# Kernel optimization log

Measured on AMD Instinct MI355X. Metric: run time of the kernel, lower is better.

Reference implementation:

```python
import jax, jax.numpy as jnp
import numpy as np

H, W, D, C = 32, 16, 16, 4
NUM_ITERS = 2
THETA_GAMMA = 3.0   # spatial (position-only) kernel bandwidth
THETA_ALPHA = 8.0   # bilateral position bandwidth
THETA_BETA = 0.5    # bilateral color bandwidth


def _attn(feats, q):
    # Gaussian-kernel attention: softmax_j(-0.5 * ||f_i - f_j||^2) @ q
    # feats: [N, F], q: [N, C] -> [N, C]
    sq = jnp.sum(feats * feats, axis=-1)
    logits = feats @ feats.T - 0.5 * (sq[:, None] + sq[None, :])  # [N, N]
    return jax.nn.softmax(logits, axis=-1) @ q


def setup_inputs() -> dict:
    key = jax.random.key(0)
    k1, k2 = jax.random.split(key)
    unaries = jax.random.normal(k1, (1, H, W, D, C), dtype=jnp.float32)
    rgb = jax.random.normal(k2, (1, H, W, D, 3), dtype=jnp.float32)
    eye = jnp.eye(C, dtype=jnp.float32)
    return {
        "unaries": unaries,
        "rgb": rgb,
        "spatial_ker_weights": eye,          # _diagonal_initializer
        "bilateral_ker_weights": eye,        # _diagonal_initializer
        "compatibility_matrix": -eye,        # _potts_model_initializer
    }


def reference(unaries, rgb, spatial_ker_weights, bilateral_ker_weights, compatibility_matrix):
    N = H * W * D
    # positions start at 1 as in tf.range(1, h+1)
    grids = jnp.meshgrid(jnp.arange(1, H + 1), jnp.arange(1, W + 1), jnp.arange(1, D + 1), indexing='ij')
    pos = jnp.stack(grids, axis=-1).astype(jnp.float32).reshape(N, 3)
    rgb_flat = rgb.reshape(N, 3)
    spatial_feats = pos / THETA_GAMMA                                             # [N, 3]
    bilateral_feats = jnp.concatenate([pos / THETA_ALPHA, rgb_flat / THETA_BETA], axis=-1)  # [N, 6]

    u = unaries.reshape(N, C)
    q = u
    for _ in range(NUM_ITERS):
        sm = jax.nn.softmax(q, axis=-1)                         # [N, C]
        spatial_out = _attn(spatial_feats, sm)                  # [N, C]
        bilateral_out = _attn(bilateral_feats, sm)              # [N, C]
        # message_passing = SK @ spatial + BK @ bilateral (class-space matmul)
        message = spatial_out @ spatial_ker_weights.T + bilateral_out @ bilateral_ker_weights.T
        pairwise = message @ compatibility_matrix.T             # [N, C]
        q = u + pairwise
    return q.reshape(unaries.shape)
```

## Files before the change

kernel.cpp:

```cpp
#include <hip/hip_runtime.h>


#define HH 32
#define WW 16
#define DDD 16
#define NN (HH * WW * DDD)
#define KS 128
#define JC (NN / KS)
#define L2E 1.4426950408889634f
#define C18 (L2E / 18.0f)
#define SQL2E 1.2011224087864498f
#define SB (SQL2E / 8.0f)
#define SC (SQL2E / 0.5f)

#if __has_builtin(__builtin_amdgcn_exp2f)
#define EXP2(x) __builtin_amdgcn_exp2f(x)
#else
#define EXP2(x) exp2f(x)
#endif

__global__ __launch_bounds__(256) void conv_dw(
    const float* __restrict__ qin,
    float* __restrict__ tmp)
{
    int h = blockIdx.x;
    int s = threadIdx.x;
    int i = h * 256 + s;

    float4 q = *((const float4*)(qin + 4 * i));
    float m = fmaxf(fmaxf(q.x, q.y), fmaxf(q.z, q.w));
    float e0 = EXP2((q.x - m) * L2E), e1 = EXP2((q.y - m) * L2E);
    float e2 = EXP2((q.z - m) * L2E), e3 = EXP2((q.w - m) * L2E);
    float rs = 1.0f / (e0 + e1 + e2 + e3);

    __shared__ float A[256][4];
    __shared__ float B[256][4];
    *((float4*)A[s]) = make_float4(e0 * rs, e1 * rs, e2 * rs, e3 * rs);
    __syncthreads();

    int w = s >> 4, d = s & 15;
    float t0 = 0, t1 = 0, t2 = 0, t3 = 0;
    #pragma unroll
    for (int dp = 0; dp < DDD; ++dp) {
        float dd = (float)(d - dp);
        float k = EXP2(-dd * dd * C18);
        const float4 v = *((const float4*)A[w * 16 + dp]);
        t0 = fmaf(k, v.x, t0); t1 = fmaf(k, v.y, t1);
        t2 = fmaf(k, v.z, t2); t3 = fmaf(k, v.w, t3);
    }
    *((float4*)B[s]) = make_float4(t0, t1, t2, t3);
    __syncthreads();

    float u0 = 0, u1 = 0, u2 = 0, u3 = 0;
    #pragma unroll
    for (int wp = 0; wp < WW; ++wp) {
        float dw = (float)(w - wp);
        float k = EXP2(-dw * dw * C18);
        const float4 v = *((const float4*)B[wp * 16 + d]);
        u0 = fmaf(k, v.x, u0); u1 = fmaf(k, v.y, u1);
        u2 = fmaf(k, v.z, u2); u3 = fmaf(k, v.w, u3);
    }
    *((float4*)(tmp + 4 * i)) = make_float4(u0, u1, u2, u3);
}

__global__ __launch_bounds__(256) void bilat_pass1(
    const float* __restrict__ qin,
    const float* __restrict__ rgb,
    float* __restrict__ part)
{
    int ib = blockIdx.x >> 7;
    int kc = blockIdx.x & (KS - 1);
    int tid = threadIdx.x;
    int i0 = ib * 1024 + tid;
    int j0 = kc * JC;

    float fw = (float)(((tid >> 4) & 15) + 1) * SB;
    float fd = (float)((tid & 15) + 1) * SB;
    int hb = i0 >> 8;
    float fh[4], cr[4][3], nn[4];
    #pragma unroll
    for (int k = 0; k < 4; ++k) {
        int ik = i0 + k * 256;
        fh[k] = (float)(hb + k + 1) * SB;
        cr[k][0] = rgb[3 * ik + 0] * SC;
        cr[k][1] = rgb[3 * ik + 1] * SC;
        cr[k][2] = rgb[3 * ik + 2] * SC;
        nn[k] = -0.5f * (fh[k] * fh[k] + fw * fw + fd * fd +
                         cr[k][0] * cr[k][0] + cr[k][1] * cr[k][1] + cr[k][2] * cr[k][2]);
    }
    float dfh[3], dc[3][3], dn[3];
    #pragma unroll
    for (int k = 0; k < 3; ++k) {
        dfh[k] = fh[k + 1] - fh[0];
        dc[k][0] = cr[k + 1][0] - cr[0][0];
        dc[k][1] = cr[k + 1][1] - cr[0][1];
        dc[k][2] = cr[k + 1][2] - cr[0][2];
        dn[k] = nn[k + 1] - nn[0];
    }

    __shared__ float recs[JC][12];
    if (tid < JC) {
        int j = j0 + tid;
        int jh = j >> 8, jr = j & 255;
        float gh = (float)(jh + 1) * SB;
        float gw = (float)((jr >> 4) + 1) * SB;
        float gd = (float)((jr & 15) + 1) * SB;
        float c0 = rgb[3 * j + 0] * SC;
        float c1 = rgb[3 * j + 1] * SC;
        float c2 = rgb[3 * j + 2] * SC;
        float nj = -0.5f * (gh * gh + gw * gw + gd * gd + c0 * c0 + c1 * c1 + c2 * c2);
        float4 q = *((const float4*)(qin + 4 * j));
        float m = fmaxf(fmaxf(q.x, q.y), fmaxf(q.z, q.w));
        float e0 = EXP2((q.x - m) * L2E), e1 = EXP2((q.y - m) * L2E);
        float e2 = EXP2((q.z - m) * L2E), e3 = EXP2((q.w - m) * L2E);
        float rs = 1.0f / (e0 + e1 + e2 + e3);
        *((float4*)&recs[tid][0]) = make_float4(gh, gw, gd, c0);
        *((float4*)&recs[tid][4]) = make_float4(c1, c2, nj, 0.0f);
        *((float4*)&recs[tid][8]) = make_float4(e0 * rs, e1 * rs, e2 * rs, e3 * rs);
    }
    __syncthreads();

    float acc[4][4];
    #pragma unroll
    for (int k = 0; k < 4; ++k)
        #pragma unroll
        for (int c = 0; c < 4; ++c) acc[k][c] = 0.0f;

    #pragma unroll 8
    for (int jj = 0; jj < JC; ++jj) {
        const float4 r0 = *((const float4*)&recs[jj][0]);
        const float4 r1 = *((const float4*)&recs[jj][4]);
        const float4 s  = *((const float4*)&recs[jj][8]);
        float g0 = nn[0] + r1.z;
        g0 = fmaf(fh[0],    r0.x, g0);
        g0 = fmaf(fw,       r0.y, g0);
        g0 = fmaf(fd,       r0.z, g0);
        g0 = fmaf(cr[0][0], r0.w, g0);
        g0 = fmaf(cr[0][1], r1.x, g0);
        g0 = fmaf(cr[0][2], r1.y, g0);
        float wk[4];
        wk[0] = EXP2(g0);
        #pragma unroll
        for (int k = 0; k < 3; ++k) {
            float g = fmaf(dfh[k], r0.x, g0 + dn[k]);
            g = fmaf(dc[k][0], r0.w, g);
            g = fmaf(dc[k][1], r1.x, g);
            g = fmaf(dc[k][2], r1.y, g);
            wk[k + 1] = EXP2(g);
        }
        #pragma unroll
        for (int k = 0; k < 4; ++k) {
            acc[k][0] = fmaf(wk[k], s.x, acc[k][0]);
            acc[k][1] = fmaf(wk[k], s.y, acc[k][1]);
            acc[k][2] = fmaf(wk[k], s.z, acc[k][2]);
            acc[k][3] = fmaf(wk[k], s.w, acc[k][3]);
        }
    }

    float* p = part + (size_t)kc * (NN * 4);
    #pragma unroll
    for (int k = 0; k < 4; ++k)
        *((float4*)(p + (size_t)(i0 + k * 256) * 4)) =
            make_float4(acc[k][0], acc[k][1], acc[k][2], acc[k][3]);
}

__global__ __launch_bounds__(256) void reduce_finish(
    const float* __restrict__ part,
    const float* __restrict__ tmp,
    const float* __restrict__ u,
    const float* __restrict__ sk, const float* __restrict__ bk,
    const float* __restrict__ cm,
    float* __restrict__ qout)
{
    int tid = threadIdx.x;
    int q = tid >> 6;
    int lane = tid & 63;
    int idx = blockIdx.x * 64 + lane;

    float bl = 0.0f;
    #pragma unroll
    for (int k = 0; k < KS / 4; ++k)
        bl += part[(size_t)(q * (KS / 4) + k) * (NN * 4) + idx];

    int i = idx >> 2;
    int h = i >> 8;
    int scid = idx & 1023;
    float sp = 0.0f;
    #pragma unroll
    for (int k = 0; k < 8; ++k) {
        int hp = q * 8 + k;
        float dh = (float)(h - hp);
        float kk = EXP2(-dh * dh * C18);
        sp = fmaf(kk, tmp[hp * 1024 + scid], sp);
    }

    __shared__ float Lb[4][64];
    __shared__ float Ls[4][64];
    Lb[q][lane] = bl;
    Ls[q][lane] = sp;
    __syncthreads();

    if (tid < 16) {
        float b4[4], s4[4];
        #pragma unroll
        for (int c = 0; c < 4; ++c) {
            int l = tid * 4 + c;
            b4[c] = Lb[0][l] + Lb[1][l] + Lb[2][l] + Lb[3][l];
            s4[c] = Ls[0][l] + Ls[1][l] + Ls[2][l] + Ls[3][l];
        }
        float rb = 1.0f / (b4[0] + b4[1] + b4[2] + b4[3]);
        float rs = 1.0f / (s4[0] + s4[1] + s4[2] + s4[3]);
        float bo[4], so[4];
        #pragma unroll
        for (int c = 0; c < 4; ++c) { bo[c] = b4[c] * rb; so[c] = s4[c] * rs; }
        float msg[4];
        #pragma unroll
        for (int c = 0; c < 4; ++c) {
            float m = 0.0f;
            #pragma unroll
            for (int d = 0; d < 4; ++d)
                m += sk[c * 4 + d] * so[d] + bk[c * 4 + d] * bo[d];
            msg[c] = m;
        }
        int ig = blockIdx.x * 16 + tid;
        #pragma unroll
        for (int c = 0; c < 4; ++c) {
            float pw = 0.0f;
            #pragma unroll
            for (int d = 0; d < 4; ++d) pw += cm[c * 4 + d] * msg[d];
            qout[4 * ig + c] = u[4 * ig + c] + pw;
        }
    }
}

extern "C" void kernel_launch(void* const* d_in, const int* in_sizes, int n_in,
                              void* d_out, int out_size, void* d_ws, size_t ws_size,
                              hipStream_t stream)
{
    const float* u   = (const float*)d_in[0];
    const float* rgb = (const float*)d_in[1];
    const float* sk  = (const float*)d_in[2];
    const float* bk  = (const float*)d_in[3];
    const float* cm  = (const float*)d_in[4];
    float* out = (float*)d_out;

    float* part = (float*)d_ws;
    float* tmpP = part + (size_t)KS * NN * 4;
    float* qbuf = tmpP + (size_t)NN * 4;

    dim3 blk(256);
    dim3 gC(HH);
    dim3 gB(8 * KS);
    dim3 gR(NN * 4 / 64);

    conv_dw<<<gC, blk, 0, stream>>>(u, tmpP);
    bilat_pass1<<<gB, blk, 0, stream>>>(u, rgb, part);
    reduce_finish<<<gR, blk, 0, stream>>>(part, tmpP, u, sk, bk, cm, qbuf);
    conv_dw<<<gC, blk, 0, stream>>>(qbuf, tmpP);
    bilat_pass1<<<gB, blk, 0, stream>>>(qbuf, rgb, part);
    reduce_finish<<<gR, blk, 0, stream>>>(part, tmpP, u, sk, bk, cm, out);
}
```

Baseline: 66.67 us.

## Fuse spatial conv and bilateral pass into one launch with smaller per-block tiles

Merges the separable spatial Gaussian conv kernel and the bilateral pairwise kernel into one launch, with the spatial work taking the tail blocks. This removes two kernel launches per run. The bilateral blocks now handle 2 query rows per thread instead of 4, doubling the grid to 2048 blocks, and the kernel adds launch bounds asking for 8 blocks per SM. This trades more redundant staging of j-records and softmax work per block for more parallelism and lower register pressure.

```diff
diff --git a/kernel.cpp b/kernel.cpp
--- a/kernel.cpp
+++ b/kernel.cpp
@@ -7,6 +7,7 @@
 #define NN (HH * WW * DDD)
 #define KS 128
 #define JC (NN / KS)
+#define GB 2048
 #define L2E 1.4426950408889634f
 #define C18 (L2E / 18.0f)
 #define SQL2E 1.2011224087864498f
@@ -19,149 +20,134 @@
 #define EXP2(x) exp2f(x)
 #endif
 
-__global__ __launch_bounds__(256) void conv_dw(
+__global__ __launch_bounds__(256, 8) void fused_bilat_conv(
     const float* __restrict__ qin,
+    const float* __restrict__ rgb,
+    float* __restrict__ part,
     float* __restrict__ tmp)
 {
-    int h = blockIdx.x;
-    int s = threadIdx.x;
-    int i = h * 256 + s;
-
-    float4 q = *((const float4*)(qin + 4 * i));
-    float m = fmaxf(fmaxf(q.x, q.y), fmaxf(q.z, q.w));
-    float e0 = EXP2((q.x - m) * L2E), e1 = EXP2((q.y - m) * L2E);
-    float e2 = EXP2((q.z - m) * L2E), e3 = EXP2((q.w - m) * L2E);
-    float rs = 1.0f / (e0 + e1 + e2 + e3);
-
-    __shared__ float A[256][4];
-    __shared__ float B[256][4];
-    *((float4*)A[s]) = make_float4(e0 * rs, e1 * rs, e2 * rs, e3 * rs);
-    __syncthreads();
-
-    int w = s >> 4, d = s & 15;
-    float t0 = 0, t1 = 0, t2 = 0, t3 = 0;
-    #pragma unroll
-    for (int dp = 0; dp < DDD; ++dp) {
-        float dd = (float)(d - dp);
-        float k = EXP2(-dd * dd * C18);
-        const float4 v = *((const float4*)A[w * 16 + dp]);
-        t0 = fmaf(k, v.x, t0); t1 = fmaf(k, v.y, t1);
-        t2 = fmaf(k, v.z, t2); t3 = fmaf(k, v.w, t3);
-    }
-    *((float4*)B[s]) = make_float4(t0, t1, t2, t3);
-    __syncthreads();
-
-    float u0 = 0, u1 = 0, u2 = 0, u3 = 0;
-    #pragma unroll
-    for (int wp = 0; wp < WW; ++wp) {
-        float dw = (float)(w - wp);
-        float k = EXP2(-dw * dw * C18);
-        const float4 v = *((const float4*)B[wp * 16 + d]);
-        u0 = fmaf(k, v.x, u0); u1 = fmaf(k, v.y, u1);
-        u2 = fmaf(k, v.z, u2); u3 = fmaf(k, v.w, u3);
-    }
-    *((float4*)(tmp + 4 * i)) = make_float4(u0, u1, u2, u3);
-}
-
-__global__ __launch_bounds__(256) void bilat_pass1(
-    const float* __restrict__ qin,
-    const float* __restrict__ rgb,
-    float* __restrict__ part)
-{
-    int ib = blockIdx.x >> 7;
-    int kc = blockIdx.x & (KS - 1);
+    __shared__ float lds[2048];
     int tid = threadIdx.x;
-    int i0 = ib * 1024 + tid;
-    int j0 = kc * JC;
-
-    float fw = (float)(((tid >> 4) & 15) + 1) * SB;
-    float fd = (float)((tid & 15) + 1) * SB;
-    int hb = i0 >> 8;
-    float fh[4], cr[4][3], nn[4];
-    #pragma unroll
-    for (int k = 0; k < 4; ++k) {
-        int ik = i0 + k * 256;
-        fh[k] = (float)(hb + k + 1) * SB;
-        cr[k][0] = rgb[3 * ik + 0] * SC;
-        cr[k][1] = rgb[3 * ik + 1] * SC;
-        cr[k][2] = rgb[3 * ik + 2] * SC;
-        nn[k] = -0.5f * (fh[k] * fh[k] + fw * fw + fd * fd +
-                         cr[k][0] * cr[k][0] + cr[k][1] * cr[k][1] + cr[k][2] * cr[k][2]);
-    }
-    float dfh[3], dc[3][3], dn[3];
-    #pragma unroll
-    for (int k = 0; k < 3; ++k) {
-        dfh[k] = fh[k + 1] - fh[0];
-        dc[k][0] = cr[k + 1][0] - cr[0][0];
-        dc[k][1] = cr[k + 1][1] - cr[0][1];
-        dc[k][2] = cr[k + 1][2] - cr[0][2];
-        dn[k] = nn[k + 1] - nn[0];
-    }
-
-    __shared__ float recs[JC][12];
-    if (tid < JC) {
-        int j = j0 + tid;
-        int jh = j >> 8, jr = j & 255;
-        float gh = (float)(jh + 1) * SB;
-        float gw = (float)((jr >> 4) + 1) * SB;
-        float gd = (float)((jr & 15) + 1) * SB;
-        float c0 = rgb[3 * j + 0] * SC;
-        float c1 = rgb[3 * j + 1] * SC;
-        float c2 = rgb[3 * j + 2] * SC;
-        float nj = -0.5f * (gh * gh + gw * gw + gd * gd + c0 * c0 + c1 * c1 + c2 * c2);
-        float4 q = *((const float4*)(qin + 4 * j));
+
+    if (blockIdx.x < GB) {
+        int ib = blockIdx.x >> 7;
+        int kc = blockIdx.x & (KS - 1);
+        int i0 = ib * 512 + tid;
+        int i1 = i0 + 256;
+        int j0 = kc * JC;
+
+        float fw = (float)(((tid >> 4) & 15) + 1) * SB;
+        float fd = (float)((tid & 15) + 1) * SB;
+        int hb = ib * 2;
+        float fh = (float)(hb + 1) * SB;
+        float c00 = rgb[3 * i0 + 0] * SC;
+        float c01 = rgb[3 * i0 + 1] * SC;
+        float c02 = rgb[3 * i0 + 2] * SC;
+        float c10 = rgb[3 * i1 + 0] * SC;
+        float c11 = rgb[3 * i1 + 1] * SC;
+        float c12 = rgb[3 * i1 + 2] * SC;
+        float fh1 = fh + SB;
+        float nn0 = -0.5f * (fh * fh + fw * fw + fd * fd +
+                             c00 * c00 + c01 * c01 + c02 * c02);
+        float nn1 = -0.5f * (fh1 * fh1 + fw * fw + fd * fd +
+                             c10 * c10 + c11 * c11 + c12 * c12);
+        float dn = nn1 - nn0;
+        float dc0 = c10 - c00, dc1 = c11 - c01, dc2 = c12 - c02;
+
+        float (*recs)[12] = (float(*)[12])lds;
+        if (tid < JC) {
+            int j = j0 + tid;
+            int jh = j >> 8, jr = j & 255;
+            float gh = (float)(jh + 1) * SB;
+            float gw = (float)((jr >> 4) + 1) * SB;
+            float gd = (float)((jr & 15) + 1) * SB;
+            float b0 = rgb[3 * j + 0] * SC;
+            float b1 = rgb[3 * j + 1] * SC;
+            float b2 = rgb[3 * j + 2] * SC;
+            float nj = -0.5f * (gh * gh + gw * gw + gd * gd +
+                                b0 * b0 + b1 * b1 + b2 * b2);
+            float4 q = *((const float4*)(qin + 4 * j));
+            float m = fmaxf(fmaxf(q.x, q.y), fmaxf(q.z, q.w));
+            float e0 = EXP2((q.x - m) * L2E), e1 = EXP2((q.y - m) * L2E);
+            float e2 = EXP2((q.z - m) * L2E), e3 = EXP2((q.w - m) * L2E);
+            float rs = 1.0f / (e0 + e1 + e2 + e3);
+            *((float4*)&recs[tid][0]) = make_float4(gh, gw, gd, b0);
+            *((float4*)&recs[tid][4]) = make_float4(b1, b2, nj, 0.0f);
+            *((float4*)&recs[tid][8]) = make_float4(e0 * rs, e1 * rs, e2 * rs, e3 * rs);
+        }
+        __syncthreads();
+
+        float a0 = 0, a1 = 0, a2 = 0, a3 = 0;
+        float b0a = 0, b1a = 0, b2a = 0, b3a = 0;
+
+        #pragma unroll 4
+        for (int jj = 0; jj < JC; ++jj) {
+            const float4 r0 = *((const float4*)&recs[jj][0]);
+            const float4 r1 = *((const float4*)&recs[jj][4]);
+            const float4 s  = *((const float4*)&recs[jj][8]);
+            float g0 = nn0 + r1.z;
+            g0 = fmaf(fh,  r0.x, g0);
+            g0 = fmaf(fw,  r0.y, g0);
+            g0 = fmaf(fd,  r0.z, g0);
+            g0 = fmaf(c00, r0.w, g0);
+            g0 = fmaf(c01, r1.x, g0);
+            g0 = fmaf(c02, r1.y, g0);
+            float g1 = g0 + dn;
+            g1 = fmaf(SB,  r0.x, g1);
+            g1 = fmaf(dc0, r0.w, g1);
+            g1 = fmaf(dc1, r1.x, g1);
+            g1 = fmaf(dc2, r1.y, g1);
+            float w0 = EXP2(g0);
+            float w1 = EXP2(g1);
+            a0  = fmaf(w0, s.x, a0);  a1  = fmaf(w0, s.y, a1);
+            a2  = fmaf(w0, s.z, a2);  a3  = fmaf(w0, s.w, a3);
+            b0a = fmaf(w1, s.x, b0a); b1a = fmaf(w1, s.y, b1a);
+            b2a = fmaf(w1, s.z, b2a); b3a = fmaf(w1, s.w, b3a);
+        }
+
+        float* p = part + (size_t)kc * (NN * 4);
+        *((float4*)(p + (size_t)i0 * 4)) = make_float4(a0, a1, a2, a3);
+        *((float4*)(p + (size_t)i1 * 4)) = make_float4(b0a, b1a, b2a, b3a);
+    } else {
+        int h = blockIdx.x - GB;
+        int s = tid;
+        int i = h * 256 + s;
+
+        float4 q = *((const float4*)(qin + 4 * i));
         float m = fmaxf(fmaxf(q.x, q.y), fmaxf(q.z, q.w));
         float e0 = EXP2((q.x - m) * L2E), e1 = EXP2((q.y - m) * L2E);
         float e2 = EXP2((q.z - m) * L2E), e3 = EXP2((q.w - m) * L2E);
         float rs = 1.0f / (e0 + e1 + e2 + e3);
-        *((float4*)&recs[tid][0]) = make_float4(gh, gw, gd, c0);
-        *((float4*)&recs[tid][4]) = make_float4(c1, c2, nj, 0.0f);
-        *((float4*)&recs[tid][8]) = make_float4(e0 * rs, e1 * rs, e2 * rs, e3 * rs);
+
+        float* A = lds;
+        float* B = lds + 1024;
+        *((float4*)(A + 4 * s)) = make_float4(e0 * rs, e1 * rs, e2 * rs, e3 * rs);
+        __syncthreads();
+
+        int w = s >> 4, d = s & 15;
+        float t0 = 0, t1 = 0, t2 = 0, t3 = 0;
+        #pragma unroll
+        for (int dp = 0; dp < DDD; ++dp) {
+            float dd = (float)(d - dp);
+            float k = EXP2(-dd * dd * C18);
+            const float4 v = *((const float4*)(A + 4 * (w * 16 + dp)));
+            t0 = fmaf(k, v.x, t0); t1 = fmaf(k, v.y, t1);
+            t2 = fmaf(k, v.z, t2); t3 = fmaf(k, v.w, t3);
+        }
+        *((float4*)(B + 4 * s)) = make_float4(t0, t1, t2, t3);
+        __syncthreads();
+
+        float u0 = 0, u1 = 0, u2 = 0, u3 = 0;
+        #pragma unroll
+        for (int wp = 0; wp < WW; ++wp) {
+            float dw = (float)(w - wp);
+            float k = EXP2(-dw * dw * C18);
+            const float4 v = *((const float4*)(B + 4 * (wp * 16 + d)));
+            u0 = fmaf(k, v.x, u0); u1 = fmaf(k, v.y, u1);
+            u2 = fmaf(k, v.z, u2); u3 = fmaf(k, v.w, u3);
+        }
+        *((float4*)(tmp + 4 * i)) = make_float4(u0, u1, u2, u3);
     }
-    __syncthreads();
-
-    float acc[4][4];
-    #pragma unroll
-    for (int k = 0; k < 4; ++k)
-        #pragma unroll
-        for (int c = 0; c < 4; ++c) acc[k][c] = 0.0f;
-
-    #pragma unroll 8
-    for (int jj = 0; jj < JC; ++jj) {
-        const float4 r0 = *((const float4*)&recs[jj][0]);
-        const float4 r1 = *((const float4*)&recs[jj][4]);
-        const float4 s  = *((const float4*)&recs[jj][8]);
-        float g0 = nn[0] + r1.z;
-        g0 = fmaf(fh[0],    r0.x, g0);
-        g0 = fmaf(fw,       r0.y, g0);
-        g0 = fmaf(fd,       r0.z, g0);
-        g0 = fmaf(cr[0][0], r0.w, g0);
-        g0 = fmaf(cr[0][1], r1.x, g0);
-        g0 = fmaf(cr[0][2], r1.y, g0);
-        float wk[4];
-        wk[0] = EXP2(g0);
-        #pragma unroll
-        for (int k = 0; k < 3; ++k) {
-            float g = fmaf(dfh[k], r0.x, g0 + dn[k]);
-            g = fmaf(dc[k][0], r0.w, g);
-            g = fmaf(dc[k][1], r1.x, g);
-            g = fmaf(dc[k][2], r1.y, g);
-            wk[k + 1] = EXP2(g);
-        }
-        #pragma unroll
-        for (int k = 0; k < 4; ++k) {
-            acc[k][0] = fmaf(wk[k], s.x, acc[k][0]);
-            acc[k][1] = fmaf(wk[k], s.y, acc[k][1]);
-            acc[k][2] = fmaf(wk[k], s.z, acc[k][2]);
-            acc[k][3] = fmaf(wk[k], s.w, acc[k][3]);
-        }
-    }
-
-    float* p = part + (size_t)kc * (NN * 4);
-    #pragma unroll
-    for (int k = 0; k < 4; ++k)
-        *((float4*)(p + (size_t)(i0 + k * 256) * 4)) =
-            make_float4(acc[k][0], acc[k][1], acc[k][2], acc[k][3]);
 }
 
 __global__ __launch_bounds__(256) void reduce_finish(
@@ -249,14 +235,11 @@
     float* qbuf = tmpP + (size_t)NN * 4;
 
     dim3 blk(256);
-    dim3 gC(HH);
-    dim3 gB(8 * KS);
+    dim3 gF(GB + HH);
     dim3 gR(NN * 4 / 64);
 
-    conv_dw<<<gC, blk, 0, stream>>>(u, tmpP);
-    bilat_pass1<<<gB, blk, 0, stream>>>(u, rgb, part);
+    fused_bilat_conv<<<gF, blk, 0, stream>>>(u, rgb, part, tmpP);
     reduce_finish<<<gR, blk, 0, stream>>>(part, tmpP, u, sk, bk, cm, qbuf);
-    conv_dw<<<gC, blk, 0, stream>>>(qbuf, tmpP);
-    bilat_pass1<<<gB, blk, 0, stream>>>(qbuf, rgb, part);
+    fused_bilat_conv<<<gF, blk, 0, stream>>>(qbuf, rgb, part, tmpP);
     reduce_finish<<<gR, blk, 0, stream>>>(part, tmpP, u, sk, bk, cm, out);
 }
```

Measured after the change: 62.36 us. -6.5%, faster.
